# Performance work log

Measured on AMD Instinct MI355X. Metric: run time of the kernel, lower is better.

The kernel has to match this reference:

```python
import jax, jax.numpy as jnp
import numpy as np

B, H, L, D = 2, 16, 2048, 64


def setup_inputs() -> dict:
    key = jax.random.key(0)
    kq, kk, kv = jax.random.split(key, 3)
    q = jax.random.normal(kq, (B, H, L, D), dtype=jnp.float32)
    k = jax.random.normal(kk, (B, H, L, D), dtype=jnp.float32)
    v = jax.random.normal(kv, (B, H, L, D), dtype=jnp.float32)
    return {"q": q, "k": k, "v": v}


def reference(q, k, v):
    use_norm = True
    seq_len = q.shape[-2]
    scale = q.shape[-1] ** (-0.5)
    q = q * scale
    # [B, H, L, L] score matrix
    attn = jnp.einsum("bhqd,bhkd->bhqk", q, k)
    # 2nd-order Taylor expansion of exp: 1 + s + 0.5*s^2
    attn = 1.0 + attn + 0.5 * attn * attn
    # causal mask (lower-triangular kept)
    causal = jnp.tril(jnp.ones((seq_len, seq_len), dtype=bool))
    attn = jnp.where(causal, attn, 0.0)
    o = jnp.einsum("bhqk,bhkd->bhqd", attn, v)
    if use_norm:
        z = attn.sum(-1)
        o = o / (z[..., None] + 1e-06)
    return o
```

## Files before the change

### kernel.cpp

```cpp
#include <hip/hip_runtime.h>
#include <hip/hip_bf16.h>

typedef __bf16    bf16x8  __attribute__((ext_vector_type(8)));
typedef __bf16    bf16x4  __attribute__((ext_vector_type(4)));
typedef _Float16  half8   __attribute__((ext_vector_type(8)));
typedef _Float16  half4   __attribute__((ext_vector_type(4)));
typedef _Float16  half2   __attribute__((ext_vector_type(2)));
typedef float     floatx4 __attribute__((ext_vector_type(4)));

constexpr int Bc  = 2;
constexpr int Hc  = 16;
constexpr int Lc  = 2048;
constexpr int Dc  = 64;
constexpr int BHn = Bc * Hc;
constexpr int BM  = 64;
constexpr int BN  = 64;
constexpr int NQT = Lc / BM;
constexpr int LDK = 72;
constexpr int LDV = 72;
constexpr int KB_T = BN * LDK * 2;
constexpr int VB_T = Dc * LDV * 2;
constexpr int TILE_BYTES = KB_T + VB_T;
constexpr int TILE_GRANS = TILE_BYTES / 16;

static __device__ __forceinline__ half2 pack_f16(float a, float b) {
    return __builtin_bit_cast(half2, __builtin_amdgcn_cvt_pkrtz(a, b));
}

static __device__ __forceinline__ void dma16(const void* g, void* l) {
    __builtin_amdgcn_global_load_lds(
        (const __attribute__((address_space(1))) void*)g,
        (__attribute__((address_space(3))) void*)l, 16, 0, 0);
}

__global__ void prep(const float* __restrict__ kp, const float* __restrict__ vp,
                     char* __restrict__ kv) {
    const int bid = blockIdx.x, tid = threadIdx.x;
    if (bid < 1024) {
        const int R    = bid * 64 + (tid >> 2);
        const int s    = tid & 3;
        const int bh   = R >> 11;
        const int key  = R & 2047;
        const int tile = key >> 6;
        const int krow = key & 63;
        const float* src = kp + (size_t)R * 64 + s * 16;
        char* dst = kv + (size_t)(bh * 32 + tile) * TILE_BYTES + krow * 144 + s * 32;
        #pragma unroll
        for (int h = 0; h < 2; ++h) {
            floatx4 a = *(const floatx4*)(src + h * 8);
            floatx4 b = *(const floatx4*)(src + h * 8 + 4);
            bf16x8 o;
            o[0] = (__bf16)a[0]; o[1] = (__bf16)a[1]; o[2] = (__bf16)a[2]; o[3] = (__bf16)a[3];
            o[4] = (__bf16)b[0]; o[5] = (__bf16)b[1]; o[6] = (__bf16)b[2]; o[7] = (__bf16)b[3];
            *(bf16x8*)(dst + h * 16) = o;
        }
    } else {
        const int vb   = bid - 1024;
        const int bh   = vb >> 5, kt = vb & 31;
        const int key  = kt * 64 + (tid & 63);
        const int kwt  = tid & 63;
        const int k5   = kwt & 31;
        const int pcol = (kwt & 32) | (((k5 >> 2) & 3) * 8 + ((k5 >> 4) & 1) * 4 + (k5 & 3));
        const int d0   = (tid >> 6) * 16;
        const float* src = vp + ((size_t)bh * Lc + key) * Dc;
        _Float16* dst = (_Float16*)(kv + (size_t)(bh * 32 + kt) * TILE_BYTES + KB_T);
        #pragma unroll
        for (int i = 0; i < 16; ++i) {
            const int d = d0 + i;
            dst[(size_t)d * LDV + pcol] = (_Float16)src[d];
        }
    }
}

__global__ __launch_bounds__(256, 4)
void taylor_attn(const float* __restrict__ qp, const char* __restrict__ kv,
                 float* __restrict__ op)
{
    __shared__ __align__(16) char smem[2 * TILE_BYTES];

    const int tid  = threadIdx.x;
    const int wv   = tid >> 6;
    const int lane = tid & 63;
    const int lm   = lane & 15;
    const int quad = lane >> 4;

    const int rnd = (int)(blockIdx.x >> 8);
    const int s_  = (int)(blockIdx.x & 255);
    const int bh  = s_ & 31;
    const int t_  = s_ >> 5;
    const int qi  = (rnd == 0) ? t_ : (rnd == 1) ? (15 - t_)
                  : (rnd == 2) ? (16 + t_) : (31 - t_);
    const int q0   = qi * BM;
    const int jmax = qi;

    const char* kvbh = kv + (size_t)bh * 32 * TILE_BYTES;

    floatx4 qv[4];
    const int r0 = tid >> 2, s4 = tid & 3;
    {
        const float* qbase = qp + ((size_t)bh * Lc + q0) * Dc;
        #pragma unroll
        for (int i = 0; i < 4; ++i)
            qv[i] = *(const floatx4*)(qbase + r0 * 64 + s4 * 16 + i * 4);
    }
    {
        #pragma unroll
        for (int rep = 0; rep < 4; ++rep)
            dma16(kvbh + (rep * 256 + tid) * 16, smem + (rep * 256 + tid) * 16);
        if (tid < 128)
            dma16(kvbh + (1024 + tid) * 16, smem + (1024 + tid) * 16);
    }

    {
        __bf16* Qs = (__bf16*)(smem + TILE_BYTES);
        #pragma unroll
        for (int i = 0; i < 4; ++i) {
            bf16x4 b;
            b[0] = (__bf16)qv[i][0]; b[1] = (__bf16)qv[i][1];
            b[2] = (__bf16)qv[i][2]; b[3] = (__bf16)qv[i][3];
            *(bf16x4*)&Qs[r0 * LDK + s4 * 16 + i * 4] = b;
        }
    }
    asm volatile("s_waitcnt lgkmcnt(0)" ::: "memory");
    __builtin_amdgcn_s_barrier();

    bf16x8 qa[2];
    {
        const __bf16* Qs = (const __bf16*)(smem + TILE_BYTES);
        #pragma unroll
        for (int kf = 0; kf < 2; ++kf)
            qa[kf] = *(const bf16x8*)&Qs[(16 * wv + lm) * LDK + kf * 32 + quad * 8];
    }
    asm volatile("s_waitcnt lgkmcnt(0)" ::: "memory");
    __builtin_amdgcn_s_barrier();

    floatx4 oacc[4] = {};
    floatx4 zacc    = {};

    const half8 ones = {(_Float16)1.f, (_Float16)1.f, (_Float16)1.f, (_Float16)1.f,
                        (_Float16)1.f, (_Float16)1.f, (_Float16)1.f, (_Float16)1.f};
    const half2 c8  = {(_Float16)0.125f, (_Float16)0.125f};
    const half2 c1  = {(_Float16)1.f,    (_Float16)1.f};
    const half2 ch  = {(_Float16)0.5f,   (_Float16)0.5f};

    for (int j = 0; j <= jmax; ++j) {
        const int cur = j & 1;
        const __bf16*   Kc = (const __bf16*)(smem + cur * TILE_BYTES);
        const _Float16* Vc = (const _Float16*)(smem + cur * TILE_BYTES + KB_T);

        if (j < jmax) {
            const char* src = kvbh + (size_t)(j + 1) * TILE_BYTES;
            char* dst = smem + (cur ^ 1) * TILE_BYTES;
            #pragma unroll
            for (int rep = 0; rep < 4; ++rep)
                dma16(src + (rep * 256 + tid) * 16, dst + (rep * 256 + tid) * 16);
            if (tid < 128)
                dma16(src + (1024 + tid) * 16, dst + (1024 + tid) * 16);
            if (wv < 2) asm volatile("s_waitcnt vmcnt(5)" ::: "memory");
            else        asm volatile("s_waitcnt vmcnt(4)" ::: "memory");
        } else {
            asm volatile("s_waitcnt vmcnt(0)" ::: "memory");
        }
        __builtin_amdgcn_s_barrier();

        floatx4 sacc[4] = {};
        #pragma unroll
        for (int kb = 0; kb < 4; ++kb) {
            #pragma unroll
            for (int kf = 0; kf < 2; ++kf) {
                bf16x8 ka = *(const bf16x8*)&Kc[(16 * kb + lm) * LDK + kf * 32 + quad * 8];
                sacc[kb] = __builtin_amdgcn_mfma_f32_16x16x32_bf16(ka, qa[kf], sacc[kb], 0, 0, 0);
            }
        }

        const bool nm = (j == jmax);
        const int  thr = 16 * wv + lm;

        half8 wf[2];
        #pragma unroll
        for (int g = 0; g < 2; ++g) {
            half2 wh[2][2];
            #pragma unroll
            for (int kb4 = 0; kb4 < 2; ++kb4) {
                const int kb = 2 * g + kb4;
                half2 s01 = pack_f16(sacc[kb][0], sacc[kb][1]);
                half2 s23 = pack_f16(sacc[kb][2], sacc[kb][3]);
                half2 a01 = s01 * c8 + c1;
                half2 a23 = s23 * c8 + c1;
                half2 w01 = a01 * (a01 * ch) + ch;
                half2 w23 = a23 * (a23 * ch) + ch;
                if (nm) {
                    const int i0 = 16 * kb + 4 * quad;
                    w01[0] = (i0 + 0 <= thr) ? w01[0] : (_Float16)0.f;
                    w01[1] = (i0 + 1 <= thr) ? w01[1] : (_Float16)0.f;
                    w23[0] = (i0 + 2 <= thr) ? w23[0] : (_Float16)0.f;
                    w23[1] = (i0 + 3 <= thr) ? w23[1] : (_Float16)0.f;
                }
                wh[kb4][0] = w01;
                wh[kb4][1] = w23;
            }
            half4 lo = __builtin_shufflevector(wh[0][0], wh[0][1], 0, 1, 2, 3);
            half4 hi = __builtin_shufflevector(wh[1][0], wh[1][1], 0, 1, 2, 3);
            wf[g] = __builtin_shufflevector(lo, hi, 0, 1, 2, 3, 4, 5, 6, 7);
        }

        #pragma unroll
        for (int db = 0; db < 4; ++db) {
            #pragma unroll
            for (int g = 0; g < 2; ++g) {
                half8 va = *(const half8*)&Vc[(16 * db + lm) * LDV + 32 * g + 8 * quad];
                oacc[db] = __builtin_amdgcn_mfma_f32_16x16x32_f16(va, wf[g], oacc[db], 0, 0, 0);
            }
        }
        #pragma unroll
        for (int g = 0; g < 2; ++g)
            zacc = __builtin_amdgcn_mfma_f32_16x16x32_f16(ones, wf[g], zacc, 0, 0, 0);

        asm volatile("s_waitcnt lgkmcnt(0)" ::: "memory");
        __builtin_amdgcn_s_barrier();
    }

    const float inv = 1.0f / (zacc[0] + 1e-6f);
    const int qrow = q0 + 16 * wv + lm;
    float* orow = op + ((size_t)bh * Lc + qrow) * Dc;
    #pragma unroll
    for (int db = 0; db < 4; ++db) {
        floatx4 t = oacc[db] * inv;
        *(floatx4*)&orow[16 * db + 4 * quad] = t;
    }
}

extern "C" void kernel_launch(void* const* d_in, const int* in_sizes, int n_in,
                              void* d_out, int out_size, void* d_ws, size_t ws_size,
                              hipStream_t stream) {
    const float* q = (const float*)d_in[0];
    const float* k = (const float*)d_in[1];
    const float* v = (const float*)d_in[2];
    float* o = (float*)d_out;

    char* kv = (char*)d_ws;

    prep<<<dim3(2048), dim3(256), 0, stream>>>(k, v, kv);
    taylor_attn<<<dim3(BHn * NQT), dim3(256), 0, stream>>>(q, kv, o);
}
```

Measured before the change: 123.8 us.

## Split key tile across wave pairs, reuse K fragments over two query strips

Each wave now covers 32 query rows and half of the 64-key tile, not 16 query rows over all keys. Every K and V fragment read from LDS feeds two MFMAs, which halves LDS read traffic per MFMA. On the diagonal tile, the wave whose key half lies entirely above its query rows skips its work. The two key-half partial outputs and normalisers are then combined through shared memory at the end, which adds an extra barrier and reduction pass and raises register pressure because accumulators double.

Measured after the change: 123.7 us. Within noise of the previous version (-0.0%).

```diff
diff --git a/kernel.cpp b/kernel.cpp
--- a/kernel.cpp
+++ b/kernel.cpp
@@ -21,7 +21,6 @@
 constexpr int KB_T = BN * LDK * 2;
 constexpr int VB_T = Dc * LDV * 2;
 constexpr int TILE_BYTES = KB_T + VB_T;
-constexpr int TILE_GRANS = TILE_BYTES / 16;
 
 static __device__ __forceinline__ half2 pack_f16(float a, float b) {
     return __builtin_bit_cast(half2, __builtin_amdgcn_cvt_pkrtz(a, b));
@@ -83,6 +82,8 @@
     const int lane = tid & 63;
     const int lm   = lane & 15;
     const int quad = lane >> 4;
+    const int wq   = wv >> 1;
+    const int wk   = wv & 1;
 
     const int rnd = (int)(blockIdx.x >> 8);
     const int s_  = (int)(blockIdx.x & 255);
@@ -124,18 +125,20 @@
     asm volatile("s_waitcnt lgkmcnt(0)" ::: "memory");
     __builtin_amdgcn_s_barrier();
 
-    bf16x8 qa[2];
+    bf16x8 qa[2][2];
     {
         const __bf16* Qs = (const __bf16*)(smem + TILE_BYTES);
         #pragma unroll
-        for (int kf = 0; kf < 2; ++kf)
-            qa[kf] = *(const bf16x8*)&Qs[(16 * wv + lm) * LDK + kf * 32 + quad * 8];
+        for (int st = 0; st < 2; ++st)
+            #pragma unroll
+            for (int kf = 0; kf < 2; ++kf)
+                qa[st][kf] = *(const bf16x8*)&Qs[(32 * wq + 16 * st + lm) * LDK + kf * 32 + quad * 8];
     }
     asm volatile("s_waitcnt lgkmcnt(0)" ::: "memory");
     __builtin_amdgcn_s_barrier();
 
-    floatx4 oacc[4] = {};
-    floatx4 zacc    = {};
+    floatx4 oacc[2][4] = {};
+    floatx4 zacc[2]    = {};
 
     const half8 ones = {(_Float16)1.f, (_Float16)1.f, (_Float16)1.f, (_Float16)1.f,
                         (_Float16)1.f, (_Float16)1.f, (_Float16)1.f, (_Float16)1.f};
@@ -163,70 +166,93 @@
         }
         __builtin_amdgcn_s_barrier();
 
-        floatx4 sacc[4] = {};
-        #pragma unroll
-        for (int kb = 0; kb < 4; ++kb) {
-            #pragma unroll
-            for (int kf = 0; kf < 2; ++kf) {
-                bf16x8 ka = *(const bf16x8*)&Kc[(16 * kb + lm) * LDK + kf * 32 + quad * 8];
-                sacc[kb] = __builtin_amdgcn_mfma_f32_16x16x32_bf16(ka, qa[kf], sacc[kb], 0, 0, 0);
-            }
-        }
-
         const bool nm = (j == jmax);
-        const int  thr = 16 * wv + lm;
-
-        half8 wf[2];
-        #pragma unroll
-        for (int g = 0; g < 2; ++g) {
-            half2 wh[2][2];
+        const bool active = !(nm && wk && !wq);
+        if (active) {
+            floatx4 sacc[2][2] = {};
             #pragma unroll
             for (int kb4 = 0; kb4 < 2; ++kb4) {
-                const int kb = 2 * g + kb4;
-                half2 s01 = pack_f16(sacc[kb][0], sacc[kb][1]);
-                half2 s23 = pack_f16(sacc[kb][2], sacc[kb][3]);
-                half2 a01 = s01 * c8 + c1;
-                half2 a23 = s23 * c8 + c1;
-                half2 w01 = a01 * (a01 * ch) + ch;
-                half2 w23 = a23 * (a23 * ch) + ch;
-                if (nm) {
-                    const int i0 = 16 * kb + 4 * quad;
-                    w01[0] = (i0 + 0 <= thr) ? w01[0] : (_Float16)0.f;
-                    w01[1] = (i0 + 1 <= thr) ? w01[1] : (_Float16)0.f;
-                    w23[0] = (i0 + 2 <= thr) ? w23[0] : (_Float16)0.f;
-                    w23[1] = (i0 + 3 <= thr) ? w23[1] : (_Float16)0.f;
+                const int row0 = 16 * (2 * wk + kb4);
+                #pragma unroll
+                for (int kf = 0; kf < 2; ++kf) {
+                    bf16x8 ka = *(const bf16x8*)&Kc[(row0 + lm) * LDK + kf * 32 + quad * 8];
+                    #pragma unroll
+                    for (int st = 0; st < 2; ++st)
+                        sacc[st][kb4] = __builtin_amdgcn_mfma_f32_16x16x32_bf16(ka, qa[st][kf], sacc[st][kb4], 0, 0, 0);
                 }
-                wh[kb4][0] = w01;
-                wh[kb4][1] = w23;
-            }
-            half4 lo = __builtin_shufflevector(wh[0][0], wh[0][1], 0, 1, 2, 3);
-            half4 hi = __builtin_shufflevector(wh[1][0], wh[1][1], 0, 1, 2, 3);
-            wf[g] = __builtin_shufflevector(lo, hi, 0, 1, 2, 3, 4, 5, 6, 7);
-        }
-
-        #pragma unroll
-        for (int db = 0; db < 4; ++db) {
-            #pragma unroll
-            for (int g = 0; g < 2; ++g) {
-                half8 va = *(const half8*)&Vc[(16 * db + lm) * LDV + 32 * g + 8 * quad];
-                oacc[db] = __builtin_amdgcn_mfma_f32_16x16x32_f16(va, wf[g], oacc[db], 0, 0, 0);
-            }
-        }
-        #pragma unroll
-        for (int g = 0; g < 2; ++g)
-            zacc = __builtin_amdgcn_mfma_f32_16x16x32_f16(ones, wf[g], zacc, 0, 0, 0);
+            }
+
+            half8 wf[2];
+            #pragma unroll
+            for (int st = 0; st < 2; ++st) {
+                const int thr = 32 * wq + 16 * st + lm;
+                half2 wh[2][2];
+                #pragma unroll
+                for (int kb4 = 0; kb4 < 2; ++kb4) {
+                    half2 s01 = pack_f16(sacc[st][kb4][0], sacc[st][kb4][1]);
+                    half2 s23 = pack_f16(sacc[st][kb4][2], sacc[st][kb4][3]);
+                    half2 a01 = s01 * c8 + c1;
+                    half2 a23 = s23 * c8 + c1;
+                    half2 w01 = a01 * (a01 * ch) + ch;
+                    half2 w23 = a23 * (a23 * ch) + ch;
+                    if (nm) {
+                        const int i0 = 16 * (2 * wk + kb4) + 4 * quad;
+                        w01[0] = (i0 + 0 <= thr) ? w01[0] : (_Float16)0.f;
+                        w01[1] = (i0 + 1 <= thr) ? w01[1] : (_Float16)0.f;
+                        w23[0] = (i0 + 2 <= thr) ? w23[0] : (_Float16)0.f;
+                        w23[1] = (i0 + 3 <= thr) ? w23[1] : (_Float16)0.f;
+                    }
+                    wh[kb4][0] = w01;
+                    wh[kb4][1] = w23;
+                }
+                half4 lo = __builtin_shufflevector(wh[0][0], wh[0][1], 0, 1, 2, 3);
+                half4 hi = __builtin_shufflevector(wh[1][0], wh[1][1], 0, 1, 2, 3);
+                wf[st] = __builtin_shufflevector(lo, hi, 0, 1, 2, 3, 4, 5, 6, 7);
+            }
+
+            #pragma unroll
+            for (int db = 0; db < 4; ++db) {
+                half8 va = *(const half8*)&Vc[(16 * db + lm) * LDV + 32 * wk + 8 * quad];
+                #pragma unroll
+                for (int st = 0; st < 2; ++st)
+                    oacc[st][db] = __builtin_amdgcn_mfma_f32_16x16x32_f16(va, wf[st], oacc[st][db], 0, 0, 0);
+            }
+            #pragma unroll
+            for (int st = 0; st < 2; ++st)
+                zacc[st] = __builtin_amdgcn_mfma_f32_16x16x32_f16(ones, wf[st], zacc[st], 0, 0, 0);
+        }
 
         asm volatile("s_waitcnt lgkmcnt(0)" ::: "memory");
         __builtin_amdgcn_s_barrier();
     }
 
-    const float inv = 1.0f / (zacc[0] + 1e-6f);
-    const int qrow = q0 + 16 * wv + lm;
-    float* orow = op + ((size_t)bh * Lc + qrow) * Dc;
-    #pragma unroll
-    for (int db = 0; db < 4; ++db) {
-        floatx4 t = oacc[db] * inv;
-        *(floatx4*)&orow[16 * db + 4 * quad] = t;
+    float* Ored = (float*)smem;
+    float* zred = (float*)(smem + 17408);
+    if (wk) {
+        #pragma unroll
+        for (int st = 0; st < 2; ++st) {
+            const int r = 32 * wq + 16 * st + lm;
+            #pragma unroll
+            for (int db = 0; db < 4; ++db)
+                *(floatx4*)&Ored[(size_t)r * 68 + 16 * db + 4 * quad] = oacc[st][db];
+            zred[r] = zacc[st][0];
+        }
+    }
+    __syncthreads();
+    if (!wk) {
+        #pragma unroll
+        for (int st = 0; st < 2; ++st) {
+            const int r = 32 * wq + 16 * st + lm;
+            const float inv = 1.0f / (zacc[st][0] + zred[r] + 1e-6f);
+            const int qrow = q0 + r;
+            float* orow = op + ((size_t)bh * Lc + qrow) * Dc;
+            #pragma unroll
+            for (int db = 0; db < 4; ++db) {
+                floatx4 part = *(const floatx4*)&Ored[(size_t)r * 68 + 16 * db + 4 * quad];
+                floatx4 t = (oacc[st][db] + part) * inv;
+                *(floatx4*)&orow[16 * db + 4 * quad] = t;
+            }
+        }
     }
 }
 
```
